# Optimization experiments

Hardware: AMD Instinct MI355X
Metric: run time of the kernel (lower is better)

The kernel has to match this reference:

```python
import jax, jax.numpy as jnp
import numpy as np

D_MODEL = 1024
NUM_HEADS = 16
B, S = 1, 4096


def setup_inputs() -> dict:
    key = jax.random.key(0)
    kx, kq, kk, kv, ko = jax.random.split(key, 5)
    std = (1.0 / D_MODEL) ** 0.5
    def trunc(k):
        return std * jax.random.truncated_normal(k, -3.0, 3.0, (D_MODEL, D_MODEL), dtype=jnp.float32)
    return {
        "x": jax.random.normal(kx, (B, S, D_MODEL), dtype=jnp.float32),
        "W_Q": trunc(kq),
        "W_K": trunc(kk),
        "W_V": trunc(kv),
        "W_O": trunc(ko),
    }


def reference(x, W_Q, W_K, W_V, W_O):
    Bx, Sx, Dm = x.shape
    H = NUM_HEADS
    d_attn = Dm // H
    # projections (torch code uses x @ W.T)
    Q = x @ W_Q.T
    K = x @ W_K.T
    V = x @ W_V.T
    # [B, H, S, d]
    Q = Q.reshape(Bx, Sx, H, d_attn).transpose(0, 2, 1, 3)
    K = K.reshape(Bx, Sx, H, d_attn).transpose(0, 2, 1, 3)
    V = V.reshape(Bx, Sx, H, d_attn).transpose(0, 2, 1, 3)
    scale = 1.0 / jnp.sqrt(jnp.asarray(d_attn, dtype=x.dtype))
    # [B, H, S, S] scores
    attn = jnp.einsum("bhqd,bhkd->bhqk", Q, K) * scale
    causal = jnp.tril(jnp.ones((Sx, Sx), dtype=bool))
    attn = jnp.where(causal, attn, jnp.asarray(-jnp.inf, dtype=attn.dtype))
    probs = jax.nn.softmax(attn, axis=-1)
    y = jnp.einsum("bhqk,bhkd->bhqd", probs, V)
    y = y.transpose(0, 2, 1, 3).reshape(Bx, Sx, Dm)
    return y @ W_O.T
```

## Files before the change

kernel.cpp:

```cpp
#include <hip/hip_runtime.h>

#define S_LEN 4096
#define DMODEL 1024
#define NHEADS 16

typedef __attribute__((ext_vector_type(8))) short bf16x8;
typedef __attribute__((ext_vector_type(4))) float f32x4;
typedef unsigned short u16;
typedef unsigned int u32;
typedef unsigned long long u64;

#define MEMFENCE asm volatile("" ::: "memory")

__device__ inline u16 f2bf(float f) {
    union { float f; u32 u; } v; v.f = f;
    u32 r = v.u + 0x7fffu + ((v.u >> 16) & 1u);
    return (u16)(r >> 16);
}

__device__ inline u32 pkbf2(float a, float b) {
    union { float f; u32 u; } ua, ub; ua.f = a; ub.f = b;
    const u32 ra = ua.u + 0x7fffu + ((ua.u >> 16) & 1u);
    const u32 rb = ub.u + 0x7fffu + ((ub.u >> 16) & 1u);
    return __builtin_amdgcn_perm(rb, ra, 0x07060302u);
}

__device__ inline u32 pkbf2f(float a, float b) {
    union { float f; u32 u; } ua, ub; ua.f = a; ub.f = b;
    const u32 ra = ua.u + 0x8000u;
    const u32 rb = ub.u + 0x8000u;
    return __builtin_amdgcn_perm(rb, ra, 0x07060302u);
}

__device__ inline void cp16(const void* g, void* l) {
    __builtin_amdgcn_global_load_lds(
        (const __attribute__((address_space(1))) unsigned int*)g,
        (__attribute__((address_space(3))) unsigned int*)l, 16, 0, 0);
}

__global__ __launch_bounds__(256) void cvt_all(const float* __restrict__ x,
                                               const float* __restrict__ wq,
                                               const float* __restrict__ wk,
                                               const float* __restrict__ wv,
                                               const float* __restrict__ wo,
                                               u16* __restrict__ xb,
                                               u16* __restrict__ w3,
                                               u16* __restrict__ wob) {
    const int b = blockIdx.x;
    const float* s; u16* d; int off;
    const int NW = DMODEL * DMODEL;
    if (b < 2048)      { s = x;  d = xb;          off = b * 2048; }
    else if (b < 2560) { s = wq; d = w3;          off = (b - 2048) * 2048; }
    else if (b < 3072) { s = wk; d = w3 + NW;     off = (b - 2560) * 2048; }
    else if (b < 3584) { s = wv; d = w3 + 2 * NW; off = (b - 3072) * 2048; }
    else               { s = wo; d = wob;         off = (b - 3584) * 2048; }
    const int i = off + threadIdx.x * 8;
    const float4 a = *(const float4*)(s + i);
    const float4 c = *(const float4*)(s + i + 4);
    u16 t[8];
    t[0] = f2bf(a.x); t[1] = f2bf(a.y); t[2] = f2bf(a.z); t[3] = f2bf(a.w);
    t[4] = f2bf(c.x); t[5] = f2bf(c.y); t[6] = f2bf(c.z); t[7] = f2bf(c.w);
    *(bf16x8*)(d + i) = *(const bf16x8*)t;
}

__global__ __launch_bounds__(256) void gemm_qkv(const u16* __restrict__ A,
                                                const u16* __restrict__ B3,
                                                u16* __restrict__ Qo,
                                                u16* __restrict__ Ko,
                                                u16* __restrict__ Vo) {
    __shared__ __align__(16) u16 As[3][128 * 32];
    __shared__ __align__(16) u16 Bs[3][128 * 32];
    const int tid = threadIdx.x, lane = tid & 63, wave = tid >> 6;
    const int wm = (wave >> 1) * 64, wn = (wave & 1) * 64;
    const int m0 = blockIdx.y * 128, n0 = blockIdx.x * 128;
    const int l15 = lane & 15, quad = lane >> 4;
    const bool swapAB = (n0 < 2048);

    f32x4 acc[4][4];
#pragma unroll
    for (int i = 0; i < 4; i++)
#pragma unroll
        for (int j = 0; j < 4; j++) acc[i][j] = (f32x4){0.f, 0.f, 0.f, 0.f};

    const int r0 = tid >> 2, c0 = (tid & 3) * 8;

#define STAGE_QKV(buf, kkb)                                                        \
    {                                                                              \
        cp16(A + (size_t)(m0 + r0) * 1024 + (kkb) + c0,       As[buf] + r0 * 32 + c0); \
        cp16(A + (size_t)(m0 + r0 + 64) * 1024 + (kkb) + c0,  As[buf] + (r0 + 64) * 32 + c0); \
        cp16(B3 + (size_t)(n0 + r0) * 1024 + (kkb) + c0,      Bs[buf] + r0 * 32 + c0); \
        cp16(B3 + (size_t)(n0 + r0 + 64) * 1024 + (kkb) + c0, Bs[buf] + (r0 + 64) * 32 + c0); \
    }

#define COMPUTE_QKV(cur)                                                           \
    {                                                                              \
        bf16x8 af[4], bfr[4];                                                      \
        _Pragma("unroll")                                                          \
        for (int i = 0; i < 4; i++)                                                \
            af[i] = *(const bf16x8*)(As[cur] + (wm + i * 16 + l15) * 32 + quad * 8); \
        _Pragma("unroll")                                                          \
        for (int j = 0; j < 4; j++)                                                \
            bfr[j] = *(const bf16x8*)(Bs[cur] + (wn + j * 16 + l15) * 32 + quad * 8); \
        if (swapAB) {                                                              \
            _Pragma("unroll")                                                      \
            for (int i = 0; i < 4; i++)                                            \
                _Pragma("unroll")                                                  \
                for (int j = 0; j < 4; j++)                                        \
                    acc[i][j] = __builtin_amdgcn_mfma_f32_16x16x32_bf16(bfr[j], af[i], acc[i][j], 0, 0, 0); \
        } else {                                                                   \
            _Pragma("unroll")                                                      \
            for (int i = 0; i < 4; i++)                                            \
                _Pragma("unroll")                                                  \
                for (int j = 0; j < 4; j++)                                        \
                    acc[i][j] = __builtin_amdgcn_mfma_f32_16x16x32_bf16(af[i], bfr[j], acc[i][j], 0, 0, 0); \
        }                                                                          \
    }

    STAGE_QKV(0, 0);
    MEMFENCE;
    STAGE_QKV(1, 32);
    MEMFENCE;

    for (int ks = 0; ks < 31; ks++) {
        asm volatile("s_waitcnt vmcnt(4)" ::: "memory");
        __builtin_amdgcn_s_barrier();
        __builtin_amdgcn_sched_barrier(0);
        if (ks < 30) {
            STAGE_QKV((ks + 2) % 3, (ks + 2) * 32);
            MEMFENCE;
        }
        COMPUTE_QKV(ks % 3);
    }
    asm volatile("s_waitcnt vmcnt(0)" ::: "memory");
    __builtin_amdgcn_s_barrier();
    __builtin_amdgcn_sched_barrier(0);
    COMPUTE_QKV(1);
#undef STAGE_QKV
#undef COMPUTE_QKV

    const int which = n0 >> 10;
    const int n0r = n0 & 1023;
    u16* dst = (which == 0) ? Qo : (which == 1) ? Ko : Vo;
    const int h = (n0r + wn) >> 6;
    u16* base = dst + (size_t)h * S_LEN * 64;
    if (which < 2) {
        const float sc = (which == 0) ? 0.125f * 1.4426950408889634f : 1.0f;
#pragma unroll
        for (int i = 0; i < 4; i++) {
            const int row = m0 + wm + i * 16 + l15;
#pragma unroll
            for (int j = 0; j < 4; j++) {
                const int c = j * 16 + quad * 4;
                const u32 y0 = pkbf2(acc[i][j][0] * sc, acc[i][j][1] * sc);
                const u32 y1 = pkbf2(acc[i][j][2] * sc, acc[i][j][3] * sc);
                *(u64*)(base + (size_t)row * 64 + c) = (u64)y0 | ((u64)y1 << 32);
            }
        }
    } else {
#pragma unroll
        for (int i = 0; i < 4; i++) {
            const int row0 = m0 + wm + i * 16 + quad * 4;
#pragma unroll
            for (int j = 0; j < 4; j++) {
                const int c = j * 16 + l15;
                const u32 y0 = pkbf2(acc[i][j][0], acc[i][j][1]);
                const u32 y1 = pkbf2(acc[i][j][2], acc[i][j][3]);
                *(u64*)(base + (size_t)c * S_LEN + row0) = (u64)y0 | ((u64)y1 << 32);
            }
        }
    }
}

__global__ __launch_bounds__(256) void gemm_out(const u16* __restrict__ A,
                                                const u16* __restrict__ B,
                                                float* __restrict__ C) {
    __shared__ __align__(16) u16 As[2][64 * 64];
    __shared__ __align__(16) u16 Bs[2][128 * 64];
    const int tid = threadIdx.x, lane = tid & 63, wave = tid >> 6;
    const int wm = (wave >> 1) * 32, wn = (wave & 1) * 64;
    const int bx = blockIdx.x;
    const int n0 = (bx & 7) * 128, m0 = (bx >> 3) * 64;
    const int l15 = lane & 15, quad = lane >> 4;
    const int swz = l15 & 7;

    f32x4 acc[2][4];
#pragma unroll
    for (int i = 0; i < 2; i++)
#pragma unroll
        for (int j = 0; j < 4; j++) acc[i][j] = (f32x4){0.f, 0.f, 0.f, 0.f};

#define STAGE_OUT(buf, kb)                                                              \
    {                                                                                   \
        _Pragma("unroll")                                                               \
        for (int q = 0; q < 2; q++) {                                                   \
            const int ch = tid + q * 256;                                               \
            const int ar = ch >> 3, ac = ((ch & 7) ^ (ar & 7)) * 8;                     \
            cp16(A + (size_t)(m0 + ar) * 1024 + (kb) + ac, As[buf] + ch * 8);           \
        }                                                                               \
        _Pragma("unroll")                                                               \
        for (int q = 0; q < 4; q++) {                                                   \
            const int ch = tid + q * 256;                                               \
            const int br = ch >> 3, bc = ((ch & 7) ^ (br & 7)) * 8;                     \
            cp16(B + (size_t)(n0 + br) * 1024 + (kb) + bc, Bs[buf] + ch * 8);           \
        }                                                                               \
    }

    STAGE_OUT(0, 0);
    int cur = 0;
    for (int kk = 0; kk < 1024; kk += 64) {
        __syncthreads();
        if (kk + 64 < 1024) STAGE_OUT(cur ^ 1, kk + 64);
#pragma unroll
        for (int h = 0; h < 2; h++) {
            const int cc = (h * 4 + quad) ^ swz;
            bf16x8 af[2], bfr[4];
#pragma unroll
            for (int i = 0; i < 2; i++)
                af[i] = *(const bf16x8*)(As[cur] + (wm + i * 16 + l15) * 64 + cc * 8);
#pragma unroll
            for (int j = 0; j < 4; j++)
                bfr[j] = *(const bf16x8*)(Bs[cur] + (wn + j * 16 + l15) * 64 + cc * 8);
#pragma unroll
            for (int i = 0; i < 2; i++)
#pragma unroll
                for (int j = 0; j < 4; j++)
                    acc[i][j] = __builtin_amdgcn_mfma_f32_16x16x32_bf16(bfr[j], af[i], acc[i][j], 0, 0, 0);
        }
        cur ^= 1;
    }
#undef STAGE_OUT

#pragma unroll
    for (int i = 0; i < 2; i++) {
        const int row = m0 + wm + i * 16 + l15;
#pragma unroll
        for (int j = 0; j < 4; j++) {
            const int col = n0 + wn + j * 16 + quad * 4;
            *(f32x4*)(C + (size_t)row * 1024 + col) = acc[i][j];
        }
    }
}

__global__ __launch_bounds__(256, 3) void attn(const u16* __restrict__ Q,
                                               const u16* __restrict__ Kh,
                                               const u16* __restrict__ Vt,
                                               u16* __restrict__ Y) {
    __shared__ __align__(16) u16 KW[2][4][2048];
    __shared__ __align__(16) u16 VW[4][2048];
    const int b = blockIdx.x;
    const int head = b & 15;
    const int jq = 63 - (b >> 4);
    const int nkt = jq + 1;
    const int np = (nkt + 1) >> 1;
    const int qa = jq * 64;
    const int tid = threadIdx.x, lane = tid & 63, w = tid >> 6;
    const int l15 = lane & 15, quad = lane >> 4;
    const int swz = l15 & 7;

    const u16* Qp = Q + (size_t)head * S_LEN * 64;
    const u16* Kp = Kh + (size_t)head * S_LEN * 64;
    const u16* Vp = Vt + (size_t)head * 64 * S_LEN;

    bf16x8 qf[4][2];
#pragma unroll
    for (int qg = 0; qg < 4; qg++)
#pragma unroll
        for (int h = 0; h < 2; h++)
            qf[qg][h] = *(const bf16x8*)(Qp + (size_t)(qa + qg * 16 + l15) * 64 + h * 32 + quad * 8);
    MEMFENCE;

    f32x4 o[4][4];
#pragma unroll
    for (int dg = 0; dg < 4; dg++)
#pragma unroll
        for (int qg = 0; qg < 4; qg++) o[dg][qg] = (f32x4){0.f, 0.f, 0.f, 0.f};
    float lp[4] = {0.f, 0.f, 0.f, 0.f};

    const int keyl = w * 16 + quad * 4;
    const int s4 = (l15 >> 1) & 3;
    const int ceo = (((quad >> 1) ^ s4)) * 8 + (quad & 1) * 4;
    const int coo = ceo ^ 16;

    union PU { u32 d[4]; bf16x8 v; };
    union VU { u64 d[2]; bf16x8 v; };

#define STAGE_K(buf, kp2)                                                               \
    {                                                                                   \
        _Pragma("unroll")                                                               \
        for (int i = 0; i < 4; i++) {                                                   \
            const int gk = (kp2) * 128 + w * 16 + (i & 1) * 8 + (lane >> 3) + (i >> 1) * 64; \
            const int lc = (lane & 7) ^ (lane >> 3);                                    \
            cp16(Kp + (size_t)gk * 64 + lc * 8, KW[buf][w] + i * 512 + lane * 8);       \
        }                                                                               \
    }

#define STAGE_V(kp2)                                                                    \
    {                                                                                   \
        _Pragma("unroll")                                                               \
        for (int i = 0; i < 4; i++) {                                                   \
            const int d = i * 16 + (lane >> 2);                                         \
            const int L = (lane & 3) ^ ((lane >> 3) & 3);                               \
            const int s = (kp2) * 128 + w * 16 + (L >> 1) * 64 + (L & 1) * 8;           \
            cp16(Vp + (size_t)d * S_LEN + s, VW[w] + i * 512 + lane * 8);               \
        }                                                                               \
    }

#define QK_PHASE(DGE, DGO, HO)                                                          \
    {                                                                                   \
        const u16* Kb = KW[cur][w];                                                     \
        const bf16x8 kE0 = *(const bf16x8*)(Kb + l15 * 64 + (quad ^ swz) * 8);          \
        const bf16x8 kE1 = *(const bf16x8*)(Kb + l15 * 64 + ((4 ^ quad) ^ swz) * 8);    \
        const bf16x8 kO0 = *(const bf16x8*)(Kb + (16 + l15) * 64 + (quad ^ swz) * 8);   \
        const bf16x8 kO1 = *(const bf16x8*)(Kb + (16 + l15) * 64 + ((4 ^ quad) ^ swz) * 8); \
        _Pragma("unroll")                                                               \
        for (int qg = 0; qg < 4; qg++) {                                                \
            const int ql = qg * 16 + l15;                                               \
            f32x4 c = (f32x4){0.f, 0.f, 0.f, 0.f};                                      \
            c = __builtin_amdgcn_mfma_f32_16x16x32_bf16(kE0, qf[qg][0], c, 0, 0, 0);    \
            c = __builtin_amdgcn_mfma_f32_16x16x32_bf16(kE1, qf[qg][1], c, 0, 0, 0);    \
            float p0 = __builtin_amdgcn_exp2f(c[0]);                                    \
            float p1 = __builtin_amdgcn_exp2f(c[1]);                                    \
            float p2 = __builtin_amdgcn_exp2f(c[2]);                                    \
            float p3 = __builtin_amdgcn_exp2f(c[3]);                                    \
            if (DGE) {                                                                  \
                if (keyl + 0 > ql) p0 = 0.f;                                            \
                if (keyl + 1 > ql) p1 = 0.f;                                            \
                if (keyl + 2 > ql) p2 = 0.f;                                            \
                if (keyl + 3 > ql) p3 = 0.f;                                            \
            }                                                                           \
            lp[qg] += (p0 + p1) + (p2 + p3);                                            \
            pu[qg].d[0] = pkbf2f(p0, p1);                                               \
            pu[qg].d[1] = pkbf2f(p2, p3);                                               \
            if (HO) {                                                                   \
                f32x4 cc = (f32x4){0.f, 0.f, 0.f, 0.f};                                 \
                cc = __builtin_amdgcn_mfma_f32_16x16x32_bf16(kO0, qf[qg][0], cc, 0, 0, 0); \
                cc = __builtin_amdgcn_mfma_f32_16x16x32_bf16(kO1, qf[qg][1], cc, 0, 0, 0); \
                float q0 = __builtin_amdgcn_exp2f(cc[0]);                               \
                float q1 = __builtin_amdgcn_exp2f(cc[1]);                               \
                float q2 = __builtin_amdgcn_exp2f(cc[2]);                               \
                float q3 = __builtin_amdgcn_exp2f(cc[3]);                               \
                if (DGO) {                                                              \
                    if (keyl + 0 > ql) q0 = 0.f;                                        \
                    if (keyl + 1 > ql) q1 = 0.f;                                        \
                    if (keyl + 2 > ql) q2 = 0.f;                                        \
                    if (keyl + 3 > ql) q3 = 0.f;                                        \
                }                                                                       \
                lp[qg] += (q0 + q1) + (q2 + q3);                                        \
                pu[qg].d[2] = pkbf2f(q0, q1);                                           \
                pu[qg].d[3] = pkbf2f(q2, q3);                                           \
            } else {                                                                    \
                pu[qg].d[2] = 0u; pu[qg].d[3] = 0u;                                     \
            }                                                                           \
        }                                                                               \
    }

#define PV_PHASE()                                                                      \
    {                                                                                   \
        _Pragma("unroll")                                                               \
        for (int dg = 0; dg < 4; dg++) {                                                \
            const u16* vb = VW[w] + (dg * 16 + l15) * 32;                               \
            VU vf;                                                                      \
            vf.d[0] = *(const u64*)(vb + ceo);                                          \
            vf.d[1] = *(const u64*)(vb + coo);                                          \
            _Pragma("unroll")                                                           \
            for (int qg = 0; qg < 4; qg++)                                              \
                o[dg][qg] = __builtin_amdgcn_mfma_f32_16x16x32_bf16(vf.v, pu[qg].v, o[dg][qg], 0, 0, 0); \
        }                                                                               \
    }

    STAGE_K(0, 0);
    MEMFENCE;
    STAGE_V(0);
    MEMFENCE;

    int cur = 0;
    for (int kp = 0; kp < np - 1; kp++) {
        STAGE_K(cur ^ 1, kp + 1);
        asm volatile("s_waitcnt vmcnt(8)" ::: "memory");
        __builtin_amdgcn_sched_barrier(0);
        PU pu[4];
        QK_PHASE(false, false, true);
        asm volatile("s_waitcnt vmcnt(4)" ::: "memory");
        __builtin_amdgcn_sched_barrier(0);
        PV_PHASE();
        MEMFENCE;
        STAGE_V(kp + 1);
        MEMFENCE;
        cur ^= 1;
    }
    {
        asm volatile("s_waitcnt vmcnt(4)" ::: "memory");
        __builtin_amdgcn_sched_barrier(0);
        const bool dE = !(jq & 1);
        const bool hO = (jq & 1);
        PU pu[4];
        QK_PHASE(dE, true, hO);
        asm volatile("s_waitcnt vmcnt(0)" ::: "memory");
        __builtin_amdgcn_sched_barrier(0);
        PV_PHASE();
    }
#undef STAGE_K
#undef STAGE_V
#undef QK_PHASE
#undef PV_PHASE

    float* OR = (float*)&KW[0][0][0];
    float* LR = (float*)((char*)&KW[0][0][0] + 24576);
#pragma unroll
    for (int qg = 0; qg < 4; qg++) {
        lp[qg] += __shfl_xor(lp[qg], 16);
        lp[qg] += __shfl_xor(lp[qg], 32);
    }
    __syncthreads();
    if (lane < 16) {
#pragma unroll
        for (int qg = 0; qg < 4; qg++) LR[(w * 4 + qg) * 16 + lane] = lp[qg];
    }
    const int qrow = tid >> 2;
    const int qgr = qrow >> 4, lq = qrow & 15;
    const int dpart = (tid & 3) * 4;
    __syncthreads();
    const float lsum = LR[qgr * 16 + lq] + LR[(4 + qgr) * 16 + lq] +
                       LR[(8 + qgr) * 16 + lq] + LR[(12 + qgr) * 16 + lq];
    const float inv = 1.f / lsum;
#pragma unroll
    for (int dg = 0; dg < 4; dg++) {
        if (dg) __syncthreads();
#pragma unroll
        for (int qg = 0; qg < 4; qg++)
            *(f32x4*)&OR[((w * 4 + qg) * 16 + l15) * 20 + quad * 4] = o[dg][qg];
        __syncthreads();
        f32x4 s = (f32x4){0.f, 0.f, 0.f, 0.f};
#pragma unroll
        for (int sw = 0; sw < 4; sw++)
            s += *(const f32x4*)&OR[((sw * 4 + qgr) * 16 + lq) * 20 + dpart];
        const u32 y0 = pkbf2(s[0] * inv, s[1] * inv);
        const u32 y1 = pkbf2(s[2] * inv, s[3] * inv);
        *(u64*)(Y + (size_t)(qa + qrow) * DMODEL + head * 64 + dg * 16 + dpart) =
            (u64)y0 | ((u64)y1 << 32);
    }
}

extern "C" void kernel_launch(void* const* d_in, const int* in_sizes, int n_in,
                              void* d_out, int out_size, void* d_ws, size_t ws_size,
                              hipStream_t stream) {
    const float* x  = (const float*)d_in[0];
    const float* wq = (const float*)d_in[1];
    const float* wk = (const float*)d_in[2];
    const float* wv = (const float*)d_in[3];
    const float* wo = (const float*)d_in[4];
    float* out = (float*)d_out;

    u16* qh  = (u16*)d_ws;
    u16* kh  = qh + (size_t)S_LEN * DMODEL;
    u16* vt  = kh + (size_t)S_LEN * DMODEL;
    u16* xb  = vt + (size_t)S_LEN * DMODEL;
    u16* y   = xb;
    u16* wb3 = xb + (size_t)S_LEN * DMODEL;
    u16* wob = wb3 + (size_t)3 * DMODEL * DMODEL;

    const dim3 blk(256);

    cvt_all<<<4096, blk, 0, stream>>>(x, wq, wk, wv, wo, xb, wb3, wob);
    gemm_qkv<<<dim3(3 * DMODEL / 128, S_LEN / 128), blk, 0, stream>>>(xb, wb3, qh, kh, vt);
    attn<<<1024, blk, 0, stream>>>(qh, kh, vt, y);
    gemm_out<<<512, blk, 0, stream>>>(y, wob, out);
}
```

Measured before the change: 211.1 us.

## Drop swapped-operand MFMA in GEMMs and add setprio around attention MFMA phases

Removes the swapAB operand swap in the QKV projection and output GEMMs and rewrites their epilogues as scalar per-element stores instead of packed 64-bit/128-bit vector stores. Adds s_setprio raise/lower around the QK and PV MFMA phases of the attention kernel so waves in compute phases get issue priority. The scalar stores give up write coalescing and vector width in the GEMM epilogues, while the priority hints target better overlap in attention.

```diff
diff --git a/kernel.cpp b/kernel.cpp
--- a/kernel.cpp
+++ b/kernel.cpp
@@ -74,7 +74,6 @@
     const int wm = (wave >> 1) * 64, wn = (wave & 1) * 64;
     const int m0 = blockIdx.y * 128, n0 = blockIdx.x * 128;
     const int l15 = lane & 15, quad = lane >> 4;
-    const bool swapAB = (n0 < 2048);
 
     f32x4 acc[4][4];
 #pragma unroll
@@ -101,19 +100,11 @@
         _Pragma("unroll")                                                          \
         for (int j = 0; j < 4; j++)                                                \
             bfr[j] = *(const bf16x8*)(Bs[cur] + (wn + j * 16 + l15) * 32 + quad * 8); \
-        if (swapAB) {                                                              \
+        _Pragma("unroll")                                                          \
+        for (int i = 0; i < 4; i++)                                                \
             _Pragma("unroll")                                                      \
-            for (int i = 0; i < 4; i++)                                            \
-                _Pragma("unroll")                                                  \
-                for (int j = 0; j < 4; j++)                                        \
-                    acc[i][j] = __builtin_amdgcn_mfma_f32_16x16x32_bf16(bfr[j], af[i], acc[i][j], 0, 0, 0); \
-        } else {                                                                   \
-            _Pragma("unroll")                                                      \
-            for (int i = 0; i < 4; i++)                                            \
-                _Pragma("unroll")                                                  \
-                for (int j = 0; j < 4; j++)                                        \
-                    acc[i][j] = __builtin_amdgcn_mfma_f32_16x16x32_bf16(af[i], bfr[j], acc[i][j], 0, 0, 0); \
-        }                                                                          \
+            for (int j = 0; j < 4; j++)                                            \
+                acc[i][j] = __builtin_amdgcn_mfma_f32_16x16x32_bf16(af[i], bfr[j], acc[i][j], 0, 0, 0); \
     }
 
     STAGE_QKV(0, 0);
@@ -141,31 +132,32 @@
     const int which = n0 >> 10;
     const int n0r = n0 & 1023;
     u16* dst = (which == 0) ? Qo : (which == 1) ? Ko : Vo;
-    const int h = (n0r + wn) >> 6;
-    u16* base = dst + (size_t)h * S_LEN * 64;
     if (which < 2) {
         const float sc = (which == 0) ? 0.125f * 1.4426950408889634f : 1.0f;
 #pragma unroll
-        for (int i = 0; i < 4; i++) {
-            const int row = m0 + wm + i * 16 + l15;
+        for (int i = 0; i < 4; i++)
 #pragma unroll
             for (int j = 0; j < 4; j++) {
-                const int c = j * 16 + quad * 4;
-                const u32 y0 = pkbf2(acc[i][j][0] * sc, acc[i][j][1] * sc);
-                const u32 y1 = pkbf2(acc[i][j][2] * sc, acc[i][j][3] * sc);
-                *(u64*)(base + (size_t)row * 64 + c) = (u64)y0 | ((u64)y1 << 32);
+                const int col = n0r + wn + j * 16 + l15;
+                const int h = col >> 6, c = col & 63;
+#pragma unroll
+                for (int r = 0; r < 4; r++) {
+                    const int row = m0 + wm + i * 16 + quad * 4 + r;
+                    dst[(size_t)h * S_LEN * 64 + (size_t)row * 64 + c] = f2bf(acc[i][j][r] * sc);
+                }
             }
-        }
     } else {
 #pragma unroll
         for (int i = 0; i < 4; i++) {
             const int row0 = m0 + wm + i * 16 + quad * 4;
 #pragma unroll
             for (int j = 0; j < 4; j++) {
-                const int c = j * 16 + l15;
+                const int col = n0r + wn + j * 16 + l15;
+                const int h = col >> 6, c = col & 63;
                 const u32 y0 = pkbf2(acc[i][j][0], acc[i][j][1]);
                 const u32 y1 = pkbf2(acc[i][j][2], acc[i][j][3]);
-                *(u64*)(base + (size_t)c * S_LEN + row0) = (u64)y0 | ((u64)y1 << 32);
+                *(u64*)(dst + (size_t)h * S_LEN * 64 + (size_t)c * S_LEN + row0) =
+                    (u64)y0 | ((u64)y1 << 32);
             }
         }
     }
@@ -224,21 +216,22 @@
             for (int i = 0; i < 2; i++)
 #pragma unroll
                 for (int j = 0; j < 4; j++)
-                    acc[i][j] = __builtin_amdgcn_mfma_f32_16x16x32_bf16(bfr[j], af[i], acc[i][j], 0, 0, 0);
+                    acc[i][j] = __builtin_amdgcn_mfma_f32_16x16x32_bf16(af[i], bfr[j], acc[i][j], 0, 0, 0);
         }
         cur ^= 1;
     }
 #undef STAGE_OUT
 
 #pragma unroll
-    for (int i = 0; i < 2; i++) {
-        const int row = m0 + wm + i * 16 + l15;
-#pragma unroll
-        for (int j = 0; j < 4; j++) {
-            const int col = n0 + wn + j * 16 + quad * 4;
-            *(f32x4*)(C + (size_t)row * 1024 + col) = acc[i][j];
-        }
-    }
+    for (int i = 0; i < 2; i++)
+#pragma unroll
+        for (int j = 0; j < 4; j++)
+#pragma unroll
+            for (int r = 0; r < 4; r++) {
+                const int row = m0 + wm + i * 16 + quad * 4 + r;
+                const int col = n0 + wn + j * 16 + l15;
+                C[(size_t)row * 1024 + col] = acc[i][j][r];
+            }
 }
 
 __global__ __launch_bounds__(256, 3) void attn(const u16* __restrict__ Q,
@@ -312,6 +305,7 @@
         const bf16x8 kE1 = *(const bf16x8*)(Kb + l15 * 64 + ((4 ^ quad) ^ swz) * 8);    \
         const bf16x8 kO0 = *(const bf16x8*)(Kb + (16 + l15) * 64 + (quad ^ swz) * 8);   \
         const bf16x8 kO1 = *(const bf16x8*)(Kb + (16 + l15) * 64 + ((4 ^ quad) ^ swz) * 8); \
+        __builtin_amdgcn_s_setprio(1);                                                  \
         _Pragma("unroll")                                                               \
         for (int qg = 0; qg < 4; qg++) {                                                \
             const int ql = qg * 16 + l15;                                               \
@@ -352,10 +346,12 @@
                 pu[qg].d[2] = 0u; pu[qg].d[3] = 0u;                                     \
             }                                                                           \
         }                                                                               \
+        __builtin_amdgcn_s_setprio(0);                                                  \
     }
 
 #define PV_PHASE()                                                                      \
     {                                                                                   \
+        __builtin_amdgcn_s_setprio(1);                                                  \
         _Pragma("unroll")                                                               \
         for (int dg = 0; dg < 4; dg++) {                                                \
             const u16* vb = VW[w] + (dg * 16 + l15) * 32;                               \
@@ -366,6 +362,7 @@
             for (int qg = 0; qg < 4; qg++)                                              \
                 o[dg][qg] = __builtin_amdgcn_mfma_f32_16x16x32_bf16(vf.v, pu[qg].v, o[dg][qg], 0, 0, 0); \
         }                                                                               \
+        __builtin_amdgcn_s_setprio(0);                                                  \
     }
 
     STAGE_K(0, 0);
```

Result: faster. 204.0 us (median of 2 runs) (-3.4%).
